# Kernel tuning notes

Hardware: AMD Instinct MI355X
Metric: run time of the kernel (lower is better)

The kernel has to match this reference:

```python
import jax, jax.numpy as jnp
import numpy as np

N, E, B = 50000, 800000, 64
IN_C, HID, HEADS = 128, 64, 4
NEG_SLOPE = 0.2


def _gat_layer(x, src, dst, W, a_src, a_dst, bias, heads, out_c, concat):
    # x: [N, F_in] -> h: [N, heads, out_c]
    h = (x @ W).reshape(-1, heads, out_c)
    alpha_src = jnp.sum(h * a_src[None], axis=-1)  # [N, heads]
    alpha_dst = jnp.sum(h * a_dst[None], axis=-1)  # [N, heads]
    e = jax.nn.leaky_relu(alpha_src[src] + alpha_dst[dst], NEG_SLOPE)  # [Etot, heads]
    # segment softmax over incoming edges of each destination node
    m = jax.lax.stop_gradient(jax.ops.segment_max(e, dst, num_segments=N))
    m = jnp.where(jnp.isfinite(m), m, 0.0)
    ex = jnp.exp(e - m[dst])
    denom = jax.ops.segment_sum(ex, dst, num_segments=N)
    alpha = ex / jnp.maximum(denom[dst], 1e-16)
    msg = h[src] * alpha[:, :, None]  # [Etot, heads, out_c]
    out = jax.ops.segment_sum(msg, dst, num_segments=N)  # [N, heads, out_c]
    if concat:
        return out.reshape(-1, heads * out_c) + bias
    return out.mean(axis=1) + bias


def setup_inputs() -> dict:
    key = jax.random.key(0)
    ks = jax.random.split(key, 16)
    g = lambda k, shp, fan: jax.random.normal(k, shp, jnp.float32) * (1.0 / np.sqrt(fan))
    return {
        "x": jax.random.normal(ks[0], (N, IN_C), jnp.float32),
        "edge_index": jax.random.randint(ks[1], (2, E), 0, N, jnp.int64),
        "batch": jnp.sort(jax.random.randint(ks[2], (N,), 0, B, jnp.int64)),
        "W1": g(ks[3], (IN_C, HEADS * HID), IN_C),
        "as1": g(ks[4], (HEADS, HID), HID),
        "ad1": g(ks[5], (HEADS, HID), HID),
        "b1": jnp.zeros((HEADS * HID,), jnp.float32),
        "W2": g(ks[6], (HEADS * HID, HEADS * HID), HEADS * HID),
        "as2": g(ks[7], (HEADS, HID), HID),
        "ad2": g(ks[8], (HEADS, HID), HID),
        "b2": jnp.zeros((HID,), jnp.float32),
        "Wm1": g(ks[9], (HID, HID), HID),
        "bm1": jnp.zeros((HID,), jnp.float32),
        "Wm2": g(ks[10], (HID, 1), HID),
        "bm2": jnp.zeros((1,), jnp.float32),
    }


def reference(x, edge_index, batch, W1, as1, ad1, b1, W2, as2, ad2, b2, Wm1, bm1, Wm2, bm2):
    # add self loops (PyG GATConv default)
    loops = jnp.arange(N, dtype=edge_index.dtype)
    src = jnp.concatenate([edge_index[0], loops])
    dst = jnp.concatenate([edge_index[1], loops])
    h = _gat_layer(x, src, dst, W1, as1, ad1, b1, HEADS, HID, concat=True)
    h = jax.nn.relu(h)
    h = _gat_layer(h, src, dst, W2, as2, ad2, b2, HEADS, HID, concat=False)
    # global mean pool over graphs
    counts = jax.ops.segment_sum(jnp.ones((N,), h.dtype), batch, num_segments=B)
    pooled = jax.ops.segment_sum(h, batch, num_segments=B) / jnp.maximum(counts, 1.0)[:, None]
    # graph MLP
    out = jax.nn.relu(pooled @ Wm1 + bm1) @ Wm2 + bm2  # [B, 1]
    return out
```

## Files before the change

kernel.cpp:

```cpp
#include <hip/hip_runtime.h>
#include <hip/hip_bf16.h>

#define N_NODES 50000
#define N_EDGES 800000
#define ETOT    (N_EDGES + N_NODES)
#define NB      64
#define IN_C    128
#define HID     64
#define HEADS   4
#define F1      (HEADS * HID)
#define NEG     0.2f
#define SCAN_NBLK ((N_NODES + 255) / 256)

typedef __attribute__((ext_vector_type(8))) short  short8v;
typedef __attribute__((ext_vector_type(4))) float  float4v;

__device__ __forceinline__ float lrelu(float x) { return x >= 0.f ? x : NEG * x; }

__device__ __forceinline__ unsigned short f2bf(float f) {
    unsigned u = __float_as_uint(f);
    u += 0x7FFFu + ((u >> 16) & 1u);
    return (unsigned short)(u >> 16);
}
__device__ __forceinline__ float bf2f(unsigned short h) {
    return __uint_as_float(((unsigned)h) << 16);
}

__global__ void deg_kernel(const int* __restrict__ ei, int* __restrict__ deg,
                           const float* __restrict__ W1,
                           unsigned short* __restrict__ W1h, unsigned short* __restrict__ W1l,
                           const float* __restrict__ W2,
                           unsigned short* __restrict__ W2h, unsigned short* __restrict__ W2l) {
    int e = blockIdx.x * 256 + threadIdx.x;
    const int N1 = IN_C * 256;
    if (e < N1) {
        int k = e >> 8, n = e & 255;
        float v = W1[e];
        unsigned short h = f2bf(v);
        W1h[n * IN_C + k] = h;
        W1l[n * IN_C + k] = f2bf(v - bf2f(h));
    } else if (e < N1 + F1 * 256) {
        int j = e - N1;
        int k = j >> 8, n = j & 255;
        float v = W2[j];
        unsigned short h = f2bf(v);
        W2h[n * F1 + k] = h;
        W2l[n * F1 + k] = f2bf(v - bf2f(h));
    }
    if (e >= ETOT) return;
    int d = (e < N_EDGES) ? ei[N_EDGES + e] : (e - N_EDGES);
    atomicAdd(&deg[d], 1);
}

__global__ void scan1_kernel(const int* __restrict__ deg, int* __restrict__ part) {
    __shared__ int sh[256];
    int t = threadIdx.x;
    int i = blockIdx.x * 256 + t;
    sh[t] = (i < N_NODES) ? deg[i] : 0;
    __syncthreads();
    #pragma unroll
    for (int o = 128; o; o >>= 1) {
        if (t < o) sh[t] += sh[t + o];
        __syncthreads();
    }
    if (t == 0) part[blockIdx.x] = sh[0];
}

__global__ void scan2_kernel(int* __restrict__ part, int* __restrict__ off) {
    __shared__ int sh[256];
    int t = threadIdx.x;
    int v = (t < SCAN_NBLK) ? part[t] : 0;
    sh[t] = v;
    __syncthreads();
    #pragma unroll
    for (int o = 1; o < 256; o <<= 1) {
        int u = (t >= o) ? sh[t - o] : 0;
        __syncthreads();
        sh[t] += u;
        __syncthreads();
    }
    if (t < SCAN_NBLK) part[t] = sh[t] - v;
    if (t == 255) off[N_NODES] = sh[255];
}

__global__ void scan3_kernel(int* __restrict__ deg, const int* __restrict__ part,
                             int* __restrict__ off) {
    __shared__ int sh[256];
    int t = threadIdx.x;
    int i = blockIdx.x * 256 + t;
    int v = (i < N_NODES) ? deg[i] : 0;
    sh[t] = v;
    __syncthreads();
    #pragma unroll
    for (int o = 1; o < 256; o <<= 1) {
        int u = (t >= o) ? sh[t - o] : 0;
        __syncthreads();
        sh[t] += u;
        __syncthreads();
    }
    if (i < N_NODES) {
        off[i] = part[blockIdx.x] + sh[t] - v;
        deg[i] = 0;
    }
}

__global__ void scatter_kernel(const int* __restrict__ ei, const int* __restrict__ off,
                               int* __restrict__ cursor, int* __restrict__ esrc) {
    int e = blockIdx.x * 256 + threadIdx.x;
    if (e >= ETOT) return;
    int s, d;
    if (e < N_EDGES) { s = ei[e]; d = ei[N_EDGES + e]; }
    else             { s = d = e - N_EDGES; }
    int pos = off[d] + atomicAdd(&cursor[d], 1);
    esrc[pos] = s;
}

template <bool SPLIT_A>
__global__ __launch_bounds__(256) void gemm_mfma(const float* __restrict__ Af32,
                                                 const unsigned short* __restrict__ Abg,
                                                 const unsigned short* __restrict__ Wth,
                                                 const unsigned short* __restrict__ Wtl,
                                                 const float* __restrict__ a_s,
                                                 const float* __restrict__ a_d,
                                                 unsigned short* __restrict__ Cb,
                                                 float* __restrict__ asrcO,
                                                 float* __restrict__ adstO,
                                                 int M, int K) {
    __shared__ unsigned short Ab[128][40];
    __shared__ unsigned short Bh[256][40], Bl[256][40];
    int t  = threadIdx.x;
    int m0 = blockIdx.x * 128;
    int w  = t >> 6, l = t & 63;
    int lr = l & 15, lk = (l >> 4) * 8;

    float asv[4], adv[4];
    #pragma unroll
    for (int nf = 0; nf < 4; ++nf) {
        asv[nf] = a_s[w * 64 + nf * 16 + lr];
        adv[nf] = a_d[w * 64 + nf * 16 + lr];
    }

    float4v acc[8][4];
    #pragma unroll
    for (int mf = 0; mf < 8; ++mf)
        #pragma unroll
        for (int nf = 0; nf < 4; ++nf)
            acc[mf][nf] = (float4v){0.f, 0.f, 0.f, 0.f};

    for (int k0 = 0; k0 < K; k0 += 32) {
        if (SPLIT_A) {
            #pragma unroll
            for (int p = 0; p < 4; ++p) {
                int idx = t + p * 256;
                int r = idx >> 3, c4 = (idx & 7) * 4;
                int gr = m0 + r;
                float4 v = make_float4(0.f, 0.f, 0.f, 0.f);
                if (gr < M) v = *(const float4*)&Af32[(size_t)gr * K + k0 + c4];
                ushort4 hi;
                hi.x = f2bf(v.x); hi.y = f2bf(v.y); hi.z = f2bf(v.z); hi.w = f2bf(v.w);
                *(ushort4*)&Ab[r][c4] = hi;
            }
        } else {
            #pragma unroll
            for (int p = 0; p < 2; ++p) {
                int idx = t + p * 256;
                int r = idx >> 2, c8 = (idx & 3) * 8;
                int gr = m0 + r;
                short8v vh = {0,0,0,0,0,0,0,0};
                if (gr < M) vh = *(const short8v*)&Abg[(size_t)gr * K + k0 + c8];
                *(short8v*)&Ab[r][c8] = vh;
            }
        }
        #pragma unroll
        for (int p = 0; p < 4; ++p) {
            int idx = t + p * 256;
            int r = idx >> 2, c8 = (idx & 3) * 8;
            short8v vh = *(const short8v*)&Wth[(size_t)r * K + k0 + c8];
            short8v vl = *(const short8v*)&Wtl[(size_t)r * K + k0 + c8];
            *(short8v*)&Bh[r][c8] = vh;
            *(short8v*)&Bl[r][c8] = vl;
        }
        __syncthreads();

        short8v b_hf[4], b_lf[4];
        #pragma unroll
        for (int nf = 0; nf < 4; ++nf) {
            b_hf[nf] = *(short8v*)&Bh[w * 64 + nf * 16 + lr][lk];
            b_lf[nf] = *(short8v*)&Bl[w * 64 + nf * 16 + lr][lk];
        }
        #pragma unroll
        for (int mf = 0; mf < 8; ++mf) {
            short8v a_f = *(short8v*)&Ab[mf * 16 + lr][lk];
            #pragma unroll
            for (int nf = 0; nf < 4; ++nf) {
                acc[mf][nf] = __builtin_amdgcn_mfma_f32_16x16x32_bf16(a_f, b_hf[nf], acc[mf][nf], 0, 0, 0);
                acc[mf][nf] = __builtin_amdgcn_mfma_f32_16x16x32_bf16(a_f, b_lf[nf], acc[mf][nf], 0, 0, 0);
            }
        }
        __syncthreads();
    }

    #pragma unroll
    for (int mf = 0; mf < 8; ++mf)
        #pragma unroll
        for (int r = 0; r < 4; ++r) {
            float ps = acc[mf][0][r] * asv[0] + acc[mf][1][r] * asv[1]
                     + acc[mf][2][r] * asv[2] + acc[mf][3][r] * asv[3];
            float pd = acc[mf][0][r] * adv[0] + acc[mf][1][r] * adv[1]
                     + acc[mf][2][r] * adv[2] + acc[mf][3][r] * adv[3];
            #pragma unroll
            for (int o = 8; o; o >>= 1) {
                ps += __shfl_xor(ps, o);
                pd += __shfl_xor(pd, o);
            }
            int gr = m0 + mf * 16 + (l >> 4) * 4 + r;
            if (lr == 0 && gr < M) {
                asrcO[gr * 4 + w] = ps;
                adstO[gr * 4 + w] = pd;
            }
        }

    #pragma unroll
    for (int mf = 0; mf < 8; ++mf)
        #pragma unroll
        for (int nf = 0; nf < 4; ++nf)
            #pragma unroll
            for (int r = 0; r < 4; ++r) {
                int gr = m0 + mf * 16 + (l >> 4) * 4 + r;
                if (gr < M) Cb[(size_t)gr * F1 + w * 64 + nf * 16 + lr] = f2bf(acc[mf][nf][r]);
            }
}

template <int LAYER>
__global__ void agg_kernel(const unsigned short* __restrict__ hb,
                           const float* __restrict__ asrc,
                           const float* __restrict__ adst,
                           const int* __restrict__ off,
                           const int* __restrict__ esrc,
                           const float* __restrict__ bias,
                           float* __restrict__ outF,
                           unsigned short* __restrict__ oh) {
    __shared__ int   soff[64];
    __shared__ float cf[64][4];
    int d    = blockIdx.x;
    int lane = threadIdx.x;
    int w    = lane >> 4;
    int e0 = off[d], e1 = off[d + 1];
    float4 ad = *(const float4*)(adst + (size_t)d * 4);
    float den = 0.f;
    float a0 = 0.f, a1 = 0.f, a2 = 0.f, a3 = 0.f;
    const char* hbase = (const char*)hb;
    int lb = lane * 8;

    for (int base = e0; base < e1; base += 64) {
        int cnt = min(64, e1 - base);
        if (lane < cnt) {
            int s = esrc[base + lane];
            soff[lane] = s * (F1 * 2);
            float4 as = *(const float4*)(asrc + (size_t)s * 4);
            cf[lane][0] = __expf(lrelu(as.x + ad.x));
            cf[lane][1] = __expf(lrelu(as.y + ad.y));
            cf[lane][2] = __expf(lrelu(as.z + ad.z));
            cf[lane][3] = __expf(lrelu(as.w + ad.w));
        }
        __syncthreads();
        int i = 0;
        for (; i + 4 <= cnt; i += 4) {
            int o0 = soff[i], o1 = soff[i + 1], o2 = soff[i + 2], o3 = soff[i + 3];
            ushort4 h0 = *(const ushort4*)(hbase + o0 + lb);
            ushort4 h1 = *(const ushort4*)(hbase + o1 + lb);
            ushort4 h2 = *(const ushort4*)(hbase + o2 + lb);
            ushort4 h3 = *(const ushort4*)(hbase + o3 + lb);
            float c0 = cf[i][w], c1 = cf[i + 1][w], c2 = cf[i + 2][w], c3 = cf[i + 3][w];
            den += (c0 + c1) + (c2 + c3);
            a0 += c0 * bf2f(h0.x) + c1 * bf2f(h1.x) + c2 * bf2f(h2.x) + c3 * bf2f(h3.x);
            a1 += c0 * bf2f(h0.y) + c1 * bf2f(h1.y) + c2 * bf2f(h2.y) + c3 * bf2f(h3.y);
            a2 += c0 * bf2f(h0.z) + c1 * bf2f(h1.z) + c2 * bf2f(h2.z) + c3 * bf2f(h3.z);
            a3 += c0 * bf2f(h0.w) + c1 * bf2f(h1.w) + c2 * bf2f(h2.w) + c3 * bf2f(h3.w);
        }
        for (; i < cnt; ++i) {
            int o = soff[i];
            float c = cf[i][w];
            ushort4 hv = *(const ushort4*)(hbase + o + lb);
            den += c;
            a0 += c * bf2f(hv.x);
            a1 += c * bf2f(hv.y);
            a2 += c * bf2f(hv.z);
            a3 += c * bf2f(hv.w);
        }
        __syncthreads();
    }

    float r = 1.f / fmaxf(den, 1e-16f);
    if (LAYER == 1) {
        ushort4 hi;
        hi.x = f2bf(fmaxf(a0 * r + bias[lane * 4 + 0], 0.f));
        hi.y = f2bf(fmaxf(a1 * r + bias[lane * 4 + 1], 0.f));
        hi.z = f2bf(fmaxf(a2 * r + bias[lane * 4 + 2], 0.f));
        hi.w = f2bf(fmaxf(a3 * r + bias[lane * 4 + 3], 0.f));
        *(ushort4*)&oh[(size_t)d * F1 + lane * 4] = hi;
    } else {
        float v0 = a0 * r, v1 = a1 * r, v2 = a2 * r, v3 = a3 * r;
        v0 += __shfl_xor(v0, 16); v0 += __shfl_xor(v0, 32);
        v1 += __shfl_xor(v1, 16); v1 += __shfl_xor(v1, 32);
        v2 += __shfl_xor(v2, 16); v2 += __shfl_xor(v2, 32);
        v3 += __shfl_xor(v3, 16); v3 += __shfl_xor(v3, 32);
        if (lane < 16) {
            float4 o;
            o.x = 0.25f * v0 + bias[lane * 4 + 0];
            o.y = 0.25f * v1 + bias[lane * 4 + 1];
            o.z = 0.25f * v2 + bias[lane * 4 + 2];
            o.w = 0.25f * v3 + bias[lane * 4 + 3];
            *(float4*)&outF[(size_t)d * HID + lane * 4] = o;
        }
    }
}

__device__ __forceinline__ int lowerb(const int* __restrict__ a, int n, int v) {
    int lo = 0, hi = n;
    while (lo < hi) { int m = (lo + hi) >> 1; if (a[m] < v) lo = m + 1; else hi = m; }
    return lo;
}

__global__ void poolmlp_kernel(const float* __restrict__ h2,
                               const int* __restrict__ batch,
                               const float* __restrict__ Wm1, const float* __restrict__ bm1,
                               const float* __restrict__ Wm2, const float* __restrict__ bm2,
                               float* __restrict__ out) {
    __shared__ float sh[4][HID];
    int b = blockIdx.x;
    int t = threadIdx.x, w = t >> 6, c = t & 63;
    int lo = lowerb(batch, N_NODES, b);
    int hi = lowerb(batch, N_NODES, b + 1);
    float s = 0.f;
    for (int n = lo + w; n < hi; n += 4) s += h2[(size_t)n * HID + c];
    sh[w][c] = s;
    __syncthreads();
    if (w == 0) {
        float inv = 1.f / fmaxf((float)(hi - lo), 1.f);
        float P = (sh[0][c] + sh[1][c] + sh[2][c] + sh[3][c]) * inv;
        sh[0][c] = P;
        float s1 = bm1[c];
        #pragma unroll
        for (int k = 0; k < HID; ++k) s1 += sh[0][k] * Wm1[k * HID + c];
        float r = fmaxf(s1, 0.f) * Wm2[c];
        #pragma unroll
        for (int o = 32; o; o >>= 1) r += __shfl_xor(r, o);
        if (c == 0) out[b] = r + bm2[0];
    }
}

extern "C" void kernel_launch(void* const* d_in, const int* in_sizes, int n_in,
                              void* d_out, int out_size, void* d_ws, size_t ws_size,
                              hipStream_t stream) {
    const float* x   = (const float*)d_in[0];
    const int*   ei  = (const int*)d_in[1];
    const int*   bat = (const int*)d_in[2];
    const float* W1  = (const float*)d_in[3];
    const float* as1 = (const float*)d_in[4];
    const float* ad1 = (const float*)d_in[5];
    const float* b1  = (const float*)d_in[6];
    const float* W2  = (const float*)d_in[7];
    const float* as2 = (const float*)d_in[8];
    const float* ad2 = (const float*)d_in[9];
    const float* b2  = (const float*)d_in[10];
    const float* Wm1 = (const float*)d_in[11];
    const float* bm1 = (const float*)d_in[12];
    const float* Wm2 = (const float*)d_in[13];
    const float* bm2 = (const float*)d_in[14];
    float* out = (float*)d_out;

    char* ws = (char*)d_ws;
    size_t cursor = 0;
    auto alloc = [&](size_t bytes) {
        void* p = ws + cursor;
        cursor += (bytes + 511) & ~(size_t)511;
        return p;
    };
    int*   deg    = (int*)alloc((size_t)N_NODES * 4);
    int*   off    = (int*)alloc((size_t)(N_NODES + 1) * 4);
    int*   part   = (int*)alloc((size_t)SCAN_NBLK * 4);
    int*   esrc   = (int*)alloc((size_t)ETOT * 4);
    unsigned short* bufHb = (unsigned short*)alloc((size_t)N_NODES * F1 * 2);
    char*  U      = (char*)alloc((size_t)N_NODES * F1 * 4);
    unsigned short* oh = (unsigned short*)U;
    float* bufO   = (float*)U;
    float* asrc   = (float*)alloc((size_t)N_NODES * HEADS * 4);
    float* adst   = (float*)alloc((size_t)N_NODES * HEADS * 4);
    unsigned short* W1th = (unsigned short*)alloc((size_t)256 * IN_C * 2);
    unsigned short* W1tl = (unsigned short*)alloc((size_t)256 * IN_C * 2);
    unsigned short* W2th = (unsigned short*)alloc((size_t)256 * F1 * 2);
    unsigned short* W2tl = (unsigned short*)alloc((size_t)256 * F1 * 2);

    hipMemsetAsync(deg, 0, (size_t)N_NODES * 4, stream);

    deg_kernel<<<(ETOT + 255) / 256, 256, 0, stream>>>(ei, deg, W1, W1th, W1tl,
                                                       W2, W2th, W2tl);
    scan1_kernel<<<SCAN_NBLK, 256, 0, stream>>>(deg, part);
    scan2_kernel<<<1, 256, 0, stream>>>(part, off);
    scan3_kernel<<<SCAN_NBLK, 256, 0, stream>>>(deg, part, off);
    scatter_kernel<<<(ETOT + 255) / 256, 256, 0, stream>>>(ei, off, deg, esrc);

    const int GB = (N_NODES + 127) / 128;
    gemm_mfma<true><<<GB, 256, 0, stream>>>(x, nullptr, W1th, W1tl,
                                            as1, ad1, bufHb, asrc, adst, N_NODES, IN_C);
    agg_kernel<1><<<N_NODES, 64, 0, stream>>>(bufHb, asrc, adst, off, esrc, b1,
                                              nullptr, oh);

    gemm_mfma<false><<<GB, 256, 0, stream>>>(nullptr, oh, W2th, W2tl,
                                             as2, ad2, bufHb, asrc, adst, N_NODES, F1);
    agg_kernel<2><<<N_NODES, 64, 0, stream>>>(bufHb, asrc, adst, off, esrc, b2,
                                              bufO, nullptr);

    poolmlp_kernel<<<NB, 256, 0, stream>>>(bufO, bat, Wm1, bm1, Wm2, bm2, out);
}
```

Before: 377.0 us.

## Pre-swizzle weights into MFMA fragment layout and load B directly from global

Weight hi/lo bf16 splits are now written in an MFMA-fragment-ordered layout, so each lane reads its B fragment straight from global or L2 memory instead of staging it through LDS. The full-K A tile is loaded into LDS once, which removes the per-k-step barriers. The row tile also shrinks from 128 to 64 to cut register use and launch more blocks. In exchange, B fragments are re-read from cache by every block, and each block does less work per B load.

```diff
diff --git a/kernel.cpp b/kernel.cpp
--- a/kernel.cpp
+++ b/kernel.cpp
@@ -24,6 +24,10 @@
 }
 __device__ __forceinline__ float bf2f(unsigned short h) {
     return __uint_as_float(((unsigned)h) << 16);
+}
+
+__device__ __forceinline__ int wf_idx(int k, int n) {
+    return (((k >> 5) * 16 + (n >> 4)) << 9) + (((k >> 3) & 3) << 7) + ((n & 15) << 3) + (k & 7);
 }
 
 __global__ void deg_kernel(const int* __restrict__ ei, int* __restrict__ deg,
@@ -37,15 +41,17 @@
         int k = e >> 8, n = e & 255;
         float v = W1[e];
         unsigned short h = f2bf(v);
-        W1h[n * IN_C + k] = h;
-        W1l[n * IN_C + k] = f2bf(v - bf2f(h));
+        int idx = wf_idx(k, n);
+        W1h[idx] = h;
+        W1l[idx] = f2bf(v - bf2f(h));
     } else if (e < N1 + F1 * 256) {
         int j = e - N1;
         int k = j >> 8, n = j & 255;
         float v = W2[j];
         unsigned short h = f2bf(v);
-        W2h[n * F1 + k] = h;
-        W2l[n * F1 + k] = f2bf(v - bf2f(h));
+        int idx = wf_idx(k, n);
+        W2h[idx] = h;
+        W2l[idx] = f2bf(v - bf2f(h));
     }
     if (e >= ETOT) return;
     int d = (e < N_EDGES) ? ei[N_EDGES + e] : (e - N_EDGES);
@@ -115,21 +121,20 @@
     esrc[pos] = s;
 }
 
-template <bool SPLIT_A>
+template <bool SPLIT_A, int K>
 __global__ __launch_bounds__(256) void gemm_mfma(const float* __restrict__ Af32,
                                                  const unsigned short* __restrict__ Abg,
-                                                 const unsigned short* __restrict__ Wth,
-                                                 const unsigned short* __restrict__ Wtl,
+                                                 const unsigned short* __restrict__ Wfh,
+                                                 const unsigned short* __restrict__ Wfl,
                                                  const float* __restrict__ a_s,
                                                  const float* __restrict__ a_d,
                                                  unsigned short* __restrict__ Cb,
                                                  float* __restrict__ asrcO,
                                                  float* __restrict__ adstO,
-                                                 int M, int K) {
-    __shared__ unsigned short Ab[128][40];
-    __shared__ unsigned short Bh[256][40], Bl[256][40];
+                                                 int M) {
+    __shared__ unsigned short Ab[64][K + 8];
     int t  = threadIdx.x;
-    int m0 = blockIdx.x * 128;
+    int m0 = blockIdx.x * 64;
     int w  = t >> 6, l = t & 63;
     int lr = l & 15, lk = (l >> 4) * 8;
 
@@ -140,68 +145,60 @@
         adv[nf] = a_d[w * 64 + nf * 16 + lr];
     }
 
-    float4v acc[8][4];
-    #pragma unroll
-    for (int mf = 0; mf < 8; ++mf)
+    {
+        int r = t >> 2, q = t & 3, gr = m0 + r;
+        if (SPLIT_A) {
+            #pragma unroll
+            for (int c = 0; c < K / 4; c += 4) {
+                int col = q * (K / 4) + c;
+                float4 v = make_float4(0.f, 0.f, 0.f, 0.f);
+                if (gr < M) v = *(const float4*)&Af32[(size_t)gr * K + col];
+                ushort4 hi;
+                hi.x = f2bf(v.x); hi.y = f2bf(v.y); hi.z = f2bf(v.z); hi.w = f2bf(v.w);
+                *(ushort4*)&Ab[r][col] = hi;
+            }
+        } else {
+            #pragma unroll
+            for (int c = 0; c < K / 4; c += 8) {
+                int col = q * (K / 4) + c;
+                short8v vh = {0,0,0,0,0,0,0,0};
+                if (gr < M) vh = *(const short8v*)&Abg[(size_t)gr * K + col];
+                *(short8v*)&Ab[r][col] = vh;
+            }
+        }
+    }
+    __syncthreads();
+
+    float4v acc[4][4];
+    #pragma unroll
+    for (int mf = 0; mf < 4; ++mf)
         #pragma unroll
         for (int nf = 0; nf < 4; ++nf)
             acc[mf][nf] = (float4v){0.f, 0.f, 0.f, 0.f};
 
-    for (int k0 = 0; k0 < K; k0 += 32) {
-        if (SPLIT_A) {
-            #pragma unroll
-            for (int p = 0; p < 4; ++p) {
-                int idx = t + p * 256;
-                int r = idx >> 3, c4 = (idx & 7) * 4;
-                int gr = m0 + r;
-                float4 v = make_float4(0.f, 0.f, 0.f, 0.f);
-                if (gr < M) v = *(const float4*)&Af32[(size_t)gr * K + k0 + c4];
-                ushort4 hi;
-                hi.x = f2bf(v.x); hi.y = f2bf(v.y); hi.z = f2bf(v.z); hi.w = f2bf(v.w);
-                *(ushort4*)&Ab[r][c4] = hi;
-            }
-        } else {
-            #pragma unroll
-            for (int p = 0; p < 2; ++p) {
-                int idx = t + p * 256;
-                int r = idx >> 2, c8 = (idx & 3) * 8;
-                int gr = m0 + r;
-                short8v vh = {0,0,0,0,0,0,0,0};
-                if (gr < M) vh = *(const short8v*)&Abg[(size_t)gr * K + k0 + c8];
-                *(short8v*)&Ab[r][c8] = vh;
-            }
-        }
-        #pragma unroll
-        for (int p = 0; p < 4; ++p) {
-            int idx = t + p * 256;
-            int r = idx >> 2, c8 = (idx & 3) * 8;
-            short8v vh = *(const short8v*)&Wth[(size_t)r * K + k0 + c8];
-            short8v vl = *(const short8v*)&Wtl[(size_t)r * K + k0 + c8];
-            *(short8v*)&Bh[r][c8] = vh;
-            *(short8v*)&Bl[r][c8] = vl;
-        }
-        __syncthreads();
-
+    constexpr int KB = K / 32;
+    #pragma unroll 2
+    for (int kb = 0; kb < KB; ++kb) {
         short8v b_hf[4], b_lf[4];
         #pragma unroll
         for (int nf = 0; nf < 4; ++nf) {
-            b_hf[nf] = *(short8v*)&Bh[w * 64 + nf * 16 + lr][lk];
-            b_lf[nf] = *(short8v*)&Bl[w * 64 + nf * 16 + lr][lk];
-        }
-        #pragma unroll
-        for (int mf = 0; mf < 8; ++mf) {
-            short8v a_f = *(short8v*)&Ab[mf * 16 + lr][lk];
+            size_t bidx = (size_t)((kb * 16 + w * 4 + nf) * 512 + l * 8);
+            b_hf[nf] = *(const short8v*)&Wfh[bidx];
+            b_lf[nf] = *(const short8v*)&Wfl[bidx];
+        }
+        #pragma unroll
+        for (int mf = 0; mf < 4; ++mf) {
+            short8v a_f = *(short8v*)&Ab[mf * 16 + lr][kb * 32 + lk];
             #pragma unroll
             for (int nf = 0; nf < 4; ++nf) {
                 acc[mf][nf] = __builtin_amdgcn_mfma_f32_16x16x32_bf16(a_f, b_hf[nf], acc[mf][nf], 0, 0, 0);
                 acc[mf][nf] = __builtin_amdgcn_mfma_f32_16x16x32_bf16(a_f, b_lf[nf], acc[mf][nf], 0, 0, 0);
             }
         }
-        __syncthreads();
-    }
-
-    #pragma unroll
-    for (int mf = 0; mf < 8; ++mf)
+    }
+
+    #pragma unroll
+    for (int mf = 0; mf < 4; ++mf)
         #pragma unroll
         for (int r = 0; r < 4; ++r) {
             float ps = acc[mf][0][r] * asv[0] + acc[mf][1][r] * asv[1]
@@ -221,7 +218,7 @@
         }
 
     #pragma unroll
-    for (int mf = 0; mf < 8; ++mf)
+    for (int mf = 0; mf < 4; ++mf)
         #pragma unroll
         for (int nf = 0; nf < 4; ++nf)
             #pragma unroll
@@ -401,14 +398,14 @@
     scan3_kernel<<<SCAN_NBLK, 256, 0, stream>>>(deg, part, off);
     scatter_kernel<<<(ETOT + 255) / 256, 256, 0, stream>>>(ei, off, deg, esrc);
 
-    const int GB = (N_NODES + 127) / 128;
-    gemm_mfma<true><<<GB, 256, 0, stream>>>(x, nullptr, W1th, W1tl,
-                                            as1, ad1, bufHb, asrc, adst, N_NODES, IN_C);
+    const int GB = (N_NODES + 63) / 64;
+    gemm_mfma<true, IN_C><<<GB, 256, 0, stream>>>(x, nullptr, W1th, W1tl,
+                                                  as1, ad1, bufHb, asrc, adst, N_NODES);
     agg_kernel<1><<<N_NODES, 64, 0, stream>>>(bufHb, asrc, adst, off, esrc, b1,
                                               nullptr, oh);
 
-    gemm_mfma<false><<<GB, 256, 0, stream>>>(nullptr, oh, W2th, W2tl,
-                                             as2, ad2, bufHb, asrc, adst, N_NODES, F1);
+    gemm_mfma<false, F1><<<GB, 256, 0, stream>>>(nullptr, oh, W2th, W2tl,
+                                                 as2, ad2, bufHb, asrc, adst, N_NODES);
     agg_kernel<2><<<N_NODES, 64, 0, stream>>>(bufHb, asrc, adst, off, esrc, b2,
                                               bufO, nullptr);
 
```

Result: faster. 362.7 us (-3.8%).
